# Kernel tuning notes

Measured on AMD Instinct MI355X. Metric: run time of the kernel, lower is better.

Reference implementation:

```python
import jax, jax.numpy as jnp
import numpy as np

D_MODEL = 1024
D_STATE = 16
D_CONV = 4
EXPAND = 2
D_INNER = EXPAND * D_MODEL
DT_RANK = D_MODEL // 16  # ceil(1024/16) = 64
BSZ = 2
SEQ = 1024


def _silu(x):
    return x * jax.nn.sigmoid(x)


def _mamba(x, in_proj, conv_w, conv_b, x_proj, dt_w, dt_b, A_log, Dp, out_proj):
    """Single-direction Mamba block. x: (B, L, d_model)."""
    Bb, Ll, _ = x.shape
    xz = jnp.einsum('bld,ed->ble', x, in_proj)          # (B,L,2*d_inner)
    xi, z = jnp.split(xz, 2, axis=-1)                   # (B,L,d_inner)
    # depthwise causal conv1d over L (kernel d_conv)
    xp = jnp.pad(xi, ((0, 0), (D_CONV - 1, 0), (0, 0)))
    xc = conv_b + sum(conv_w[:, k] * xp[:, k:k + Ll, :] for k in range(D_CONV))
    xc = _silu(xc)                                      # (B,L,d_inner)
    dbl = jnp.einsum('ble,fe->blf', xc, x_proj)         # (B,L,dt_rank+2*d_state)
    dt, Bm, Cm = jnp.split(dbl, [DT_RANK, DT_RANK + D_STATE], axis=-1)
    delta = jax.nn.softplus(jnp.einsum('blr,er->ble', dt, dt_w) + dt_b)  # (B,L,d_inner)
    A = -jnp.exp(A_log)                                 # (d_inner,d_state)
    dA = jnp.exp(delta[..., None] * A)                  # (B,L,E,N)
    dBu = (delta * xc)[..., None] * Bm[:, :, None, :]   # (B,L,E,N)
    def step(h, t):
        dA_t, dBu_t, C_t = t
        h = dA_t * h + dBu_t                            # (B,E,N)
        return h, jnp.einsum('ben,bn->be', h, C_t)
    h0 = jnp.zeros((Bb, D_INNER, D_STATE), x.dtype)
    _, ys = jax.lax.scan(step, h0, (dA.transpose(1, 0, 2, 3),
                                    dBu.transpose(1, 0, 2, 3),
                                    Cm.transpose(1, 0, 2)))
    y = ys.transpose(1, 0, 2) + xc * Dp                 # skip connection
    y = y * _silu(z)                                    # gate
    return jnp.einsum('ble,de->bld', y, out_proj)


def setup_inputs() -> dict:
    key = jax.random.key(0)
    ks = jax.random.split(key, 4)
    def nrm(k, shape, s=0.02):
        return s * jax.random.normal(k, shape, dtype=jnp.float32)
    def mamba_params(kb):
        k = jax.random.split(kb, 6)
        return dict(
            in_proj=nrm(k[0], (2 * D_INNER, D_MODEL)),
            conv_w=nrm(k[1], (D_INNER, D_CONV), 0.2),
            conv_b=jnp.zeros((D_INNER,), jnp.float32),
            x_proj=nrm(k[2], (DT_RANK + 2 * D_STATE, D_INNER)),
            dt_w=nrm(k[3], (D_INNER, DT_RANK), 0.1),
            dt_b=nrm(k[4], (D_INNER,), 0.5) - 4.0,  # softplus -> dt ~ 0.018
            A_log=jnp.log(jnp.broadcast_to(jnp.arange(1, D_STATE + 1, dtype=jnp.float32), (D_INNER, D_STATE))),
            D=jnp.ones((D_INNER,), jnp.float32),
            out_proj=nrm(k[5], (D_MODEL, D_INNER)),
        )
    inp = {'x': jax.random.normal(ks[2], (BSZ, SEQ, D_MODEL), dtype=jnp.float32)}
    for name, p in (('fwd', mamba_params(ks[0])), ('bwd', mamba_params(ks[1]))):
        for kk, v in p.items():
            inp[f'{name}_{kk}'] = v
    inp['merge_w'] = nrm(ks[3], (D_MODEL, 2 * D_MODEL))
    return inp


def reference(x,
              fwd_in_proj, fwd_conv_w, fwd_conv_b, fwd_x_proj, fwd_dt_w, fwd_dt_b,
              fwd_A_log, fwd_D, fwd_out_proj,
              bwd_in_proj, bwd_conv_w, bwd_conv_b, bwd_x_proj, bwd_dt_w, bwd_dt_b,
              bwd_A_log, bwd_D, bwd_out_proj,
              merge_w):
    f = _mamba(x, fwd_in_proj, fwd_conv_w, fwd_conv_b, fwd_x_proj, fwd_dt_w,
               fwd_dt_b, fwd_A_log, fwd_D, fwd_out_proj)
    b = _mamba(jnp.flip(x, 1), bwd_in_proj, bwd_conv_w, bwd_conv_b, bwd_x_proj,
               bwd_dt_w, bwd_dt_b, bwd_A_log, bwd_D, bwd_out_proj)
    b = jnp.flip(b, 1)
    return jnp.einsum('blf,df->bld', jnp.concatenate([f, b], axis=-1), merge_w)
```

## Files before the change

### kernel.cpp

```cpp
#include <hip/hip_runtime.h>
#include <math.h>

#define BSZ 2
#define SEQ 1024
#define DM  1024
#define DI  2048
#define DS  16
#define DC  4
#define DR  64
#define NDBL 96
#define NC  32
#define LC  32
#define MM  (BSZ * SEQ)

typedef unsigned short u16;
typedef __bf16 bf16x8 __attribute__((ext_vector_type(8)));
typedef float  f32x4  __attribute__((ext_vector_type(4)));

constexpr int N4_X   = MM * DM / 4;
constexpr int N4_MW  = DM * 2 * DM / 4;
constexpr int N4_IN  = 2 * DI * DM / 4;
constexpr int N4_XP  = NDBL * DI / 4;
constexpr int N4_DT  = DI * DR / 4;
constexpr int N4_OUT = DM * DI / 4;
constexpr int N4_TOTAL = N4_X + N4_MW + 2 * (N4_IN + N4_XP + N4_DT + N4_OUT);
constexpr size_t O_XP  = (size_t)2 * DI * DM;
constexpr size_t O_DT  = O_XP + (size_t)NDBL * DI;
constexpr size_t O_OUT = O_DT + (size_t)DI * DR;
constexpr size_t WBF_SZ = O_OUT + (size_t)DM * DI;

__device__ __forceinline__ u16 f2b(float f) {
    unsigned int u = __float_as_uint(f);
    unsigned int r = (u + 0x7fffu + ((u >> 16) & 1u)) >> 16;
    return (u16)r;
}
__device__ __forceinline__ float b2f(u16 h) {
    return __uint_as_float(((unsigned int)h) << 16);
}

__device__ __forceinline__ void stf(float* p, size_t i, float v) { p[i] = v; }
__device__ __forceinline__ void stf(u16* p, size_t i, float v)   { p[i] = f2b(v); }

__device__ __forceinline__ float fexp(float x)  { return __expf(x); }
__device__ __forceinline__ float frcp(float x)  { return __builtin_amdgcn_rcpf(x); }
__device__ __forceinline__ float silu_fast(float x) {
    return x * frcp(1.f + fexp(-x));
}
__device__ __forceinline__ float softplus_fast(float x) {
    return (x > 15.f) ? x : __logf(1.f + fexp(x));
}

__device__ __forceinline__ void async16(const u16* g, u16* l) {
    __builtin_amdgcn_global_load_lds(
        (const __attribute__((address_space(1))) void*)g,
        (__attribute__((address_space(3))) void*)l, 16, 0, 0);
}

__device__ __forceinline__ int lds_slot(int row, int j) {
    return row * 4 + ((j + (row >> 1)) & 3);
}

__device__ __forceinline__ void stage8f(const float* p, u16* d) {
    float4 v0 = *(const float4*)p;
    float4 v1 = *(const float4*)(p + 4);
    ushort4 a; a.x = f2b(v0.x); a.y = f2b(v0.y); a.z = f2b(v0.z); a.w = f2b(v0.w);
    ushort4 b; b.x = f2b(v1.x); b.y = f2b(v1.y); b.z = f2b(v1.z); b.w = f2b(v1.w);
    *(ushort4*)d = a;
    *(ushort4*)(d + 4) = b;
}

__global__ __launch_bounds__(256) void cvt_all_kernel(
    const float* __restrict__ s0, const float* __restrict__ s1,
    const float* __restrict__ s2, const float* __restrict__ s3,
    const float* __restrict__ s4, const float* __restrict__ s5,
    const float* __restrict__ s6, const float* __restrict__ s7,
    const float* __restrict__ s8, const float* __restrict__ s9,
    u16* __restrict__ d0, u16* __restrict__ d1, u16* __restrict__ d2,
    u16* __restrict__ d3, u16* __restrict__ d4, u16* __restrict__ d5,
    u16* __restrict__ d6, u16* __restrict__ d7, u16* __restrict__ d8,
    u16* __restrict__ d9)
{
    int i = blockIdx.x * 256 + threadIdx.x;
    const float* s; u16* d;
    if (i < N4_X) { s = s0; d = d0; }
    else if ((i -= N4_X) < N4_MW) { s = s1; d = d1; }
    else if ((i -= N4_MW) < N4_IN) { s = s2; d = d2; }
    else if ((i -= N4_IN) < N4_XP) { s = s3; d = d3; }
    else if ((i -= N4_XP) < N4_DT) { s = s4; d = d4; }
    else if ((i -= N4_DT) < N4_OUT) { s = s5; d = d5; }
    else if ((i -= N4_OUT) < N4_IN) { s = s6; d = d6; }
    else if ((i -= N4_IN) < N4_XP) { s = s7; d = d7; }
    else if ((i -= N4_XP) < N4_DT) { s = s8; d = d8; }
    else if ((i -= N4_DT) < N4_OUT) { s = s9; d = d9; }
    else return;
    float4 v = ((const float4*)s)[i];
    ushort4 o; o.x = f2b(v.x); o.y = f2b(v.y); o.z = f2b(v.z); o.w = f2b(v.w);
    ((ushort4*)d)[i] = o;
}

template <typename TA, typename TC, int ACT, bool DUAL, bool FLIP1, int NSPLIT, int BN>
__global__ __launch_bounds__(256) void mfma_gemm(
    const TA* __restrict__ A0, const TA* __restrict__ A1, int lda,
    const u16* __restrict__ W0, const u16* __restrict__ W1, int ldw,
    const float* __restrict__ bias0, const float* __restrict__ bias1,
    TC* __restrict__ C0, TC* __restrict__ C1, int ldc,
    int M, int N, int K)
{
    constexpr int NF = BN / 32;
    __shared__ u16 As[128 * 32];
    __shared__ u16 Ws[BN * 32];

    const int z = blockIdx.z;
    const int dir = DUAL ? (z / NSPLIT) : 0;
    const int split = z % NSPLIT;
    const TA* A = dir ? A1 : A0;
    const u16* W = dir ? W1 : W0;
    const float* bias = dir ? bias1 : bias0;
    TC* C = dir ? C1 : C0;
    if (NSPLIT > 1) C += (size_t)split * M * ldc;
    const int kseg = K / NSPLIT;
    const int kbeg = split * kseg, kend = kbeg + kseg;

    const int t = threadIdx.x;
    const int wave = t >> 6;
    const int lane = t & 63;
    const int wm = (wave & 1) * 64;
    const int wn = (wave >> 1) * (BN / 2);
    const int fm = lane & 15;
    const int q  = lane >> 4;
    const int m0 = blockIdx.y * 128;
    const int n0 = blockIdx.x * BN;

    f32x4 acc[4][NF] = {};

    for (int k0 = kbeg; k0 < kend; k0 += 32) {
        if constexpr (__is_same(TA, u16)) {
            #pragma unroll
            for (int p = 0; p < 2; p++) {
                int i = p * 256 + wave * 64 + lane;
                int r = i >> 2;
                int j = ((i & 3) - (r >> 1)) & 3;
                async16(A + (size_t)(m0 + r) * lda + k0 + j * 8,
                        &As[(size_t)(p * 256 + wave * 64) * 8]);
            }
        } else {
            #pragma unroll
            for (int p = 0; p < 2; p++) {
                int i = p * 256 + t;
                int r = i >> 2;
                int j = ((i & 3) - (r >> 1)) & 3;
                stage8f(A + (size_t)(m0 + r) * lda + k0 + j * 8, &As[(size_t)i * 8]);
            }
        }
        #pragma unroll
        for (int p = 0; p < BN / 64; p++) {
            int i = p * 256 + wave * 64 + lane;
            int r = i >> 2;
            int j = ((i & 3) - (r >> 1)) & 3;
            int gr = n0 + r;
            if (gr >= N) gr = N - 1;
            async16(W + (size_t)gr * ldw + k0 + j * 8,
                    &Ws[(size_t)(p * 256 + wave * 64) * 8]);
        }
        __syncthreads();

        bf16x8 af[4], wf[NF];
        #pragma unroll
        for (int mi = 0; mi < 4; mi++)
            af[mi] = *(const bf16x8*)&As[(size_t)lds_slot(wm + mi * 16 + fm, q) * 8];
        #pragma unroll
        for (int ni = 0; ni < NF; ni++)
            wf[ni] = *(const bf16x8*)&Ws[(size_t)lds_slot(wn + ni * 16 + fm, q) * 8];
        #pragma unroll
        for (int mi = 0; mi < 4; mi++)
            #pragma unroll
            for (int ni = 0; ni < NF; ni++)
                acc[mi][ni] = __builtin_amdgcn_mfma_f32_16x16x32_bf16(
                    af[mi], wf[ni], acc[mi][ni], 0, 0, 0);
        __syncthreads();
    }

    const int rb = q * 4;
    const int cc = fm;
    #pragma unroll
    for (int mi = 0; mi < 4; mi++) {
        #pragma unroll
        for (int r = 0; r < 4; r++) {
            int gm = m0 + wm + mi * 16 + rb + r;
            int om = gm;
            if (FLIP1 && dir == 1) {
                int bb = gm / SEQ, l = gm % SEQ;
                om = bb * SEQ + (SEQ - 1 - l);
            }
            #pragma unroll
            for (int ni = 0; ni < NF; ni++) {
                int gn = n0 + wn + ni * 16 + cc;
                if (gn < N) {
                    float v = acc[mi][ni][r];
                    if (ACT == 1) v = softplus_fast(v + bias[gn]);
                    stf(C, (size_t)om * ldc + gn, v);
                }
            }
        }
    }
}

__global__ __launch_bounds__(256) void combine_dbl_kernel(
    const float* __restrict__ par, float* __restrict__ dbl)
{
    int i4 = blockIdx.x * 256 + threadIdx.x;
    const int per = (MM * NDBL) / 4;
    int dir = (i4 >= per) ? 1 : 0;
    int j4 = i4 - dir * per;
    const float* p = par + (size_t)dir * 4 * MM * NDBL;
    f32x4 s = {0.f, 0.f, 0.f, 0.f};
    #pragma unroll
    for (int k = 0; k < 4; k++)
        s += *(const f32x4*)&p[(size_t)k * MM * NDBL + (size_t)j4 * 4];
    *(f32x4*)&dbl[(size_t)dir * MM * NDBL + (size_t)j4 * 4] = s;
}

__global__ __launch_bounds__(256) void combine_cat_kernel(
    const float* __restrict__ par, u16* __restrict__ cat)
{
    int i4 = blockIdx.x * 256 + threadIdx.x;
    const int per = (MM * DM) / 4;
    int dir = (i4 >= per) ? 1 : 0;
    int j4 = i4 - dir * per;
    const float* p0 = par + (size_t)dir * 2 * MM * DM;
    const float* p1 = p0 + (size_t)MM * DM;
    f32x4 a = *(const f32x4*)&p0[(size_t)j4 * 4];
    f32x4 b = *(const f32x4*)&p1[(size_t)j4 * 4];
    int m = j4 >> 8;
    int n4 = j4 & 255;
    ushort4 o;
    o.x = f2b(a[0] + b[0]); o.y = f2b(a[1] + b[1]);
    o.z = f2b(a[2] + b[2]); o.w = f2b(a[3] + b[3]);
    *(ushort4*)&cat[(size_t)m * 2 * DM + dir * DM + n4 * 4] = o;
}

__global__ __launch_bounds__(256) void combine_out_kernel(
    const float* __restrict__ p0, float* __restrict__ out)
{
    int i4 = blockIdx.x * 256 + threadIdx.x;
    const float* p1 = p0 + (size_t)MM * DM;
    f32x4 a = *(const f32x4*)&p0[(size_t)i4 * 4];
    f32x4 b = *(const f32x4*)&p1[(size_t)i4 * 4];
    *(f32x4*)&out[(size_t)i4 * 4] = a + b;
}

__global__ __launch_bounds__(256) void conv_silu_kernel(
    const float* __restrict__ xz,
    const float* __restrict__ cw0, const float* __restrict__ cw1,
    const float* __restrict__ cb0, const float* __restrict__ cb1,
    u16* __restrict__ xcb)
{
    int i4 = blockIdx.x * 256 + threadIdx.x;
    const int per = MM * DI / 4;
    int dir = (i4 >= per) ? 1 : 0;
    int rem = i4 - dir * per;
    int e4 = rem & (DI / 4 - 1);
    int bl = rem / (DI / 4);
    int l = bl & (SEQ - 1);
    int e = e4 * 4;
    const float* xz_d = xz + (size_t)dir * MM * 2 * DI;
    const float* cw = dir ? cw1 : cw0;
    const float* cb = dir ? cb1 : cb0;
    f32x4 cwv[4];
    #pragma unroll
    for (int i = 0; i < 4; i++) cwv[i] = *(const f32x4*)&cw[(e + i) * DC];
    f32x4 acc = *(const f32x4*)&cb[e];
    #pragma unroll
    for (int k = 0; k < DC; k++) {
        int ll = l + k - (DC - 1);
        if (ll >= 0) {
            f32x4 xv = *(const f32x4*)&xz_d[(size_t)(bl - l + ll) * (2 * DI) + e];
            #pragma unroll
            for (int i = 0; i < 4; i++) acc[i] += cwv[i][k] * xv[i];
        }
    }
    ushort4 o;
    #pragma unroll
    for (int i = 0; i < 4; i++) {
        float s = silu_fast(acc[i]);
        ((u16*)&o)[i] = f2b(s);
    }
    ((ushort4*)xcb)[(size_t)dir * per + rem] = o;
}

__global__ __launch_bounds__(256) void scan_pass1(
    const float* __restrict__ dbl,
    const u16*  __restrict__ xc,
    const u16*  __restrict__ delta,
    const float* __restrict__ Alog0, const float* __restrict__ Alog1,
    float* __restrict__ Pout, float* __restrict__ Qout)
{
    __shared__ float sB[LC][16];
    const int t = threadIdx.x;
    const int c = blockIdx.x;
    const int dir = blockIdx.z >> 1;
    const int b = blockIdx.z & 1;
    const int e = blockIdx.y * 256 + t;
    const int row0 = b * SEQ + c * LC;
    const float* dbl_d = dbl + (size_t)dir * MM * NDBL;
    const u16* xc_d = xc + (size_t)dir * MM * DI;
    const u16* delta_d = delta + (size_t)dir * MM * DI;
    const float* A_log = dir ? Alog1 : Alog0;
    float* P_d = Pout + (size_t)dir * BSZ * NC * DI * DS;
    float* Q_d = Qout + (size_t)dir * BSZ * NC * DI * DS;

    if (t < LC * 4) {
        int row = t >> 2, col = (t & 3) * 4;
        *(f32x4*)&sB[row][col] =
            *(const f32x4*)&dbl_d[(size_t)(row0 + row) * NDBL + DR + col];
    }

    f32x4 Aen[4], P[4], Q[4];
    #pragma unroll
    for (int g = 0; g < 4; g++) {
        f32x4 a = *(const f32x4*)&A_log[(size_t)e * DS + g * 4];
        #pragma unroll
        for (int j = 0; j < 4; j++) Aen[g][j] = -fexp(a[j]);
        P[g] = f32x4{1.f, 1.f, 1.f, 1.f};
        Q[g] = f32x4{0.f, 0.f, 0.f, 0.f};
    }
    __syncthreads();

    float dv = b2f(delta_d[(size_t)row0 * DI + e]);
    float xv = b2f(xc_d[(size_t)row0 * DI + e]);
    for (int i = 0; i < LC; i++) {
        int ip = (i + 1 < LC) ? (i + 1) : (LC - 1);
        float dvn = b2f(delta_d[(size_t)(row0 + ip) * DI + e]);
        float xvn = b2f(xc_d[(size_t)(row0 + ip) * DI + e]);
        float du = dv * xv;
        #pragma unroll
        for (int g = 0; g < 4; g++) {
            f32x4 Bv = *(const f32x4*)&sB[i][g * 4];
            #pragma unroll
            for (int j = 0; j < 4; j++) {
                float dA = fexp(dv * Aen[g][j]);
                P[g][j] *= dA;
                Q[g][j] = dA * Q[g][j] + du * Bv[j];
            }
        }
        dv = dvn; xv = xvn;
    }
    size_t base = ((size_t)(b * NC + c) * DI + e) * DS;
    #pragma unroll
    for (int g = 0; g < 4; g++) {
        *(f32x4*)&P_d[base + g * 4] = P[g];
        *(f32x4*)&Q_d[base + g * 4] = Q[g];
    }
}

__global__ __launch_bounds__(256) void scan_pass2(
    const float* __restrict__ P, const float* __restrict__ Q,
    float* __restrict__ H0)
{
    const int gid = blockIdx.x * 256 + threadIdx.x;
    const int dir = gid >> 16;
    const int loc = gid & 65535;
    const int b = loc >> 15;
    const int en = loc & (DI * DS - 1);
    size_t doff = (size_t)dir * BSZ * NC * DI * DS;
    float h = 0.f;
    for (int c = 0; c < NC; c++) {
        size_t idx = doff + ((size_t)(b * NC + c) * DI * DS) + en;
        H0[idx] = h;
        h = P[idx] * h + Q[idx];
    }
}

__global__ __launch_bounds__(256) void scan_pass3(
    const float* __restrict__ dbl,
    const u16*  __restrict__ xc,
    const float* __restrict__ xz,
    u16* delta_y,
    const float* __restrict__ Alog0, const float* __restrict__ Alog1,
    const float* __restrict__ Dp0, const float* __restrict__ Dp1,
    const float* __restrict__ H0)
{
    __shared__ float sBC[LC][32];
    const int t = threadIdx.x;
    const int c = blockIdx.x;
    const int dir = blockIdx.z >> 1;
    const int b = blockIdx.z & 1;
    const int e = blockIdx.y * 256 + t;
    const int row0 = b * SEQ + c * LC;
    const float* dbl_d = dbl + (size_t)dir * MM * NDBL;
    const u16* xc_d = xc + (size_t)dir * MM * DI;
    const float* xz_d = xz + (size_t)dir * MM * 2 * DI;
    u16* dy_d = delta_y + (size_t)dir * MM * DI;
    const float* A_log = dir ? Alog1 : Alog0;
    const float* Dp = dir ? Dp1 : Dp0;
    const float* H0_d = H0 + (size_t)dir * BSZ * NC * DI * DS;

    {
        int row = t >> 3, col = (t & 7) * 4;
        *(f32x4*)&sBC[row][col] =
            *(const f32x4*)&dbl_d[(size_t)(row0 + row) * NDBL + DR + col];
    }

    f32x4 Aen[4], h[4];
    size_t base = ((size_t)(b * NC + c) * DI + e) * DS;
    #pragma unroll
    for (int g = 0; g < 4; g++) {
        f32x4 a = *(const f32x4*)&A_log[(size_t)e * DS + g * 4];
        #pragma unroll
        for (int j = 0; j < 4; j++) Aen[g][j] = -fexp(a[j]);
        h[g] = *(const f32x4*)&H0_d[base + g * 4];
    }
    const float Dv = Dp[e];
    __syncthreads();

    float dv = b2f(dy_d[(size_t)row0 * DI + e]);
    float xv = b2f(xc_d[(size_t)row0 * DI + e]);
    float zv = xz_d[(size_t)row0 * (2 * DI) + DI + e];
    for (int i = 0; i < LC; i++) {
        int ip = (i + 1 < LC) ? (i + 1) : (LC - 1);
        float dvn = b2f(dy_d[(size_t)(row0 + ip) * DI + e]);
        float xvn = b2f(xc_d[(size_t)(row0 + ip) * DI + e]);
        float zvn = xz_d[(size_t)(row0 + ip) * (2 * DI) + DI + e];
        float du = dv * xv;
        f32x4 pv = {0.f, 0.f, 0.f, 0.f};
        #pragma unroll
        for (int g = 0; g < 4; g++) {
            f32x4 Bv = *(const f32x4*)&sBC[i][g * 4];
            f32x4 Cv = *(const f32x4*)&sBC[i][16 + g * 4];
            #pragma unroll
            for (int j = 0; j < 4; j++) {
                float dA = fexp(dv * Aen[g][j]);
                h[g][j] = dA * h[g][j] + du * Bv[j];
                pv[j] += h[g][j] * Cv[j];
            }
        }
        float p = pv[0] + pv[1] + pv[2] + pv[3];
        float y = (p + xv * Dv) * silu_fast(zv);
        dy_d[(size_t)(row0 + i) * DI + e] = f2b(y);
        dv = dvn; xv = xvn; zv = zvn;
    }
}

extern "C" void kernel_launch(void* const* d_in, const int* in_sizes, int n_in,
                              void* d_out, int out_size, void* d_ws, size_t ws_size,
                              hipStream_t stream)
{
    const float* x = (const float*)d_in[0];
    const float* in_p[2]  = {(const float*)d_in[1],  (const float*)d_in[10]};
    const float* conv_w[2]= {(const float*)d_in[2],  (const float*)d_in[11]};
    const float* conv_b[2]= {(const float*)d_in[3],  (const float*)d_in[12]};
    const float* x_p[2]   = {(const float*)d_in[4],  (const float*)d_in[13]};
    const float* dt_w[2]  = {(const float*)d_in[5],  (const float*)d_in[14]};
    const float* dt_b[2]  = {(const float*)d_in[6],  (const float*)d_in[15]};
    const float* A_log[2] = {(const float*)d_in[7],  (const float*)d_in[16]};
    const float* Dp[2]    = {(const float*)d_in[8],  (const float*)d_in[17]};
    const float* out_p[2] = {(const float*)d_in[9],  (const float*)d_in[18]};
    const float* merge_w  = (const float*)d_in[19];
    float* out = (float*)d_out;

    float* ws = (float*)d_ws;
    float* ws_xz  = ws;
    float* ws_dbl = ws_xz  + (size_t)2 * MM * 2 * DI;
    float* ws_P   = ws_dbl + (size_t)2 * MM * NDBL;
    float* ws_Q   = ws_P   + (size_t)2 * BSZ * NC * DI * DS;
    float* ws_H0  = ws_Q   + (size_t)2 * BSZ * NC * DI * DS;
    u16* ws_delta = (u16*)(ws_H0 + (size_t)2 * BSZ * NC * DI * DS);
    u16* ws_xcb   = ws_delta + (size_t)2 * MM * DI;
    u16* ws_cat   = ws_xcb   + (size_t)2 * MM * DI;
    u16* ws_xbf   = ws_cat   + (size_t)MM * 2 * DM;
    u16* wbf_mw   = ws_xbf   + (size_t)MM * DM;
    u16* wbf0     = wbf_mw   + (size_t)DM * 2 * DM;
    u16* wbf1     = wbf0     + WBF_SZ;
    float* ws_par = ws_P;

    cvt_all_kernel<<<(N4_TOTAL + 255) / 256, 256, 0, stream>>>(
        x, merge_w, in_p[0], x_p[0], dt_w[0], out_p[0],
        in_p[1], x_p[1], dt_w[1], out_p[1],
        ws_xbf, wbf_mw,
        wbf0, wbf0 + O_XP, wbf0 + O_DT, wbf0 + O_OUT,
        wbf1, wbf1 + O_XP, wbf1 + O_DT, wbf1 + O_OUT);

    mfma_gemm<u16, float, 0, true, true, 1, 128><<<dim3(32, 16, 2), 256, 0, stream>>>(
        ws_xbf, ws_xbf, DM, wbf0, wbf1, DM, nullptr, nullptr,
        ws_xz, ws_xz + (size_t)MM * 2 * DI, 2 * DI, MM, 2 * DI, DM);

    conv_silu_kernel<<<(2 * MM * DI / 4) / 256, 256, 0, stream>>>(
        ws_xz, conv_w[0], conv_w[1], conv_b[0], conv_b[1], ws_xcb);

    mfma_gemm<u16, float, 0, true, false, 4, 64><<<dim3(2, 16, 8), 256, 0, stream>>>(
        ws_xcb, ws_xcb + (size_t)MM * DI, DI,
        wbf0 + O_XP, wbf1 + O_XP, DI, nullptr, nullptr,
        ws_par, ws_par + (size_t)4 * MM * NDBL, NDBL, MM, NDBL, DI);
    combine_dbl_kernel<<<(2 * MM * NDBL / 4) / 256, 256, 0, stream>>>(ws_par, ws_dbl);

    mfma_gemm<float, u16, 1, true, false, 1, 64><<<dim3(32, 16, 2), 256, 0, stream>>>(
        ws_dbl, ws_dbl + (size_t)MM * NDBL, NDBL,
        wbf0 + O_DT, wbf1 + O_DT, DR, dt_b[0], dt_b[1],
        ws_delta, ws_delta + (size_t)MM * DI, DI, MM, DI, DR);

    {
        dim3 grid(NC, DI / 256, 2 * BSZ);
        scan_pass1<<<grid, 256, 0, stream>>>(ws_dbl, ws_xcb, ws_delta,
                                             A_log[0], A_log[1], ws_P, ws_Q);
        scan_pass2<<<(2 * BSZ * DI * DS) / 256, 256, 0, stream>>>(ws_P, ws_Q, ws_H0);
        scan_pass3<<<grid, 256, 0, stream>>>(ws_dbl, ws_xcb, ws_xz, ws_delta,
                                             A_log[0], A_log[1], Dp[0], Dp[1], ws_H0);
    }

    mfma_gemm<u16, float, 0, true, true, 2, 64><<<dim3(16, 16, 4), 256, 0, stream>>>(
        ws_delta, ws_delta + (size_t)MM * DI, DI,
        wbf0 + O_OUT, wbf1 + O_OUT, DI, nullptr, nullptr,
        ws_par, ws_par + (size_t)2 * MM * DM, DM, MM, DM, DI);
    combine_cat_kernel<<<(2 * MM * DM / 4) / 256, 256, 0, stream>>>(ws_par, ws_cat);

    mfma_gemm<u16, float, 0, false, false, 2, 64><<<dim3(16, 16, 2), 256, 0, stream>>>(
        ws_cat, ws_cat, 2 * DM, wbf_mw, wbf_mw, 2 * DM, nullptr, nullptr,
        ws_par, ws_par, DM, MM, DM, 2 * DM);
    combine_out_kernel<<<(MM * DM / 4) / 256, 256, 0, stream>>>(ws_par, out);
}
```

Measured before the change: 395.8 us.

## Replace in_proj GEMM with 256x256-tile double-buffered async-LDS MFMA kernel

Adds a dedicated in_proj GEMM kernel that uses 256x256 output tiles, 512 threads, 128 KB of LDS with swizzled layout, async global-to-LDS loads and double buffering interleaved with 16x16x32 bf16 MFMAs. It is meant to raise operand reuse and overlap loads with math compared to the older 128-wide tile GEMM for the largest projection. The tradeoff is that only 256 blocks are launched, which may underfill the GPU. Heavy LDS use also limits occupancy to one block per CU, and the manual waitcnt schedule is fragile.

```diff
diff --git a/kernel.cpp b/kernel.cpp
--- a/kernel.cpp
+++ b/kernel.cpp
@@ -98,6 +98,179 @@
     ((ushort4*)d)[i] = o;
 }
 
+__global__ __launch_bounds__(512) void gemm256_dual(
+    const u16* __restrict__ A,
+    const u16* __restrict__ Wd0, const u16* __restrict__ Wd1,
+    float* __restrict__ Cd0, float* __restrict__ Cd1,
+    int lda, int ldw, int ldc, int K)
+{
+    __shared__ u16 lds[65536];
+    const int t    = threadIdx.x;
+    const int lane = t & 63;
+    const int w    = t >> 6;
+    const int wr   = w >> 2;
+    const int wc   = w & 3;
+    const int fm   = lane & 15;
+    const int q    = lane >> 4;
+    const int dir  = blockIdx.z;
+    const u16* W   = dir ? Wd1 : Wd0;
+    float* C       = dir ? Cd1 : Cd0;
+    const int m0   = blockIdx.y * 256;
+    const int n0   = blockIdx.x * 256;
+    const int T    = K >> 6;
+
+    int offA[4][2], offW[2][2];
+    #pragma unroll
+    for (int mi = 0; mi < 4; mi++)
+        #pragma unroll
+        for (int kk = 0; kk < 2; kk++) {
+            int r = wr * 64 + mi * 16 + fm;
+            int j = kk * 4 + q;
+            offA[mi][kk] = (r * 8 + ((j + r) & 7)) * 8;
+        }
+    #pragma unroll
+    for (int ni = 0; ni < 2; ni++)
+        #pragma unroll
+        for (int kk = 0; kk < 2; kk++) {
+            int r = wc * 32 + ni * 16 + fm;
+            int j = kk * 4 + q;
+            offW[ni][kk] = (r * 8 + ((j + r) & 7)) * 8;
+        }
+
+    int sr[2], sj[2];
+    #pragma unroll
+    for (int p = 0; p < 2; p++) {
+        int slot = p * 512 + t;
+        sr[p] = slot >> 3;
+        sj[p] = ((slot & 7) - sr[p]) & 7;
+    }
+    const int ldsWaveBase = (t & ~63) * 8;
+
+#define STAGE(G, ld, row0, kcol, dstBase)                                    \
+    { _Pragma("unroll")                                                      \
+      for (int p = 0; p < 2; p++) {                                          \
+          const u16* src_ = (G) + (size_t)((row0) + sr[p]) * (ld)            \
+                          + (kcol) + sj[p] * 8;                              \
+          async16(src_, &lds[(dstBase) + p * 4096 + ldsWaveBase]);           \
+      } }
+
+    f32x4 acc[2][2][4][2] = {};
+    bf16x8 af[4][2], wf[2][2];
+
+#define DSREAD_A(mh, cur)                                                    \
+    { _Pragma("unroll")                                                      \
+      for (int mi = 0; mi < 4; mi++)                                         \
+          _Pragma("unroll")                                                  \
+          for (int kk = 0; kk < 2; kk++)                                     \
+              af[mi][kk] = *(const bf16x8*)&lds[(cur) + (mh) * 8192          \
+                                                + offA[mi][kk]]; }
+#define DSREAD_W(nh, cur)                                                    \
+    { _Pragma("unroll")                                                      \
+      for (int ni = 0; ni < 2; ni++)                                         \
+          _Pragma("unroll")                                                  \
+          for (int kk = 0; kk < 2; kk++)                                     \
+              wf[ni][kk] = *(const bf16x8*)&lds[(cur) + 16384 + (nh) * 8192  \
+                                                + offW[ni][kk]]; }
+#define MFMA16(mh, nh)                                                       \
+    { __builtin_amdgcn_s_setprio(1);                                         \
+      _Pragma("unroll")                                                      \
+      for (int mi = 0; mi < 4; mi++)                                         \
+          _Pragma("unroll")                                                  \
+          for (int ni = 0; ni < 2; ni++)                                     \
+              _Pragma("unroll")                                              \
+              for (int kk = 0; kk < 2; kk++)                                 \
+                  acc[mh][nh][mi][ni] =                                      \
+                      __builtin_amdgcn_mfma_f32_16x16x32_bf16(               \
+                          af[mi][kk], wf[ni][kk], acc[mh][nh][mi][ni],       \
+                          0, 0, 0);                                          \
+      __builtin_amdgcn_s_setprio(0); }
+
+#define WAITVM(n) asm volatile("s_waitcnt vmcnt(" #n ")" ::: "memory")
+#define BAR() __builtin_amdgcn_s_barrier()
+
+    STAGE(A, lda, m0,       0, 0);
+    STAGE(W, ldw, n0,       0, 16384);
+    STAGE(W, ldw, n0 + 128, 0, 16384 + 8192);
+    STAGE(A, lda, m0 + 128, 0, 8192);
+    WAITVM(4);
+    BAR();
+
+    for (int tt = 0; tt < T - 1; ++tt) {
+        const int cur = (tt & 1) * 32768;
+        const int nxt = 32768 - cur;
+        const int kn  = (tt + 1) << 6;
+        DSREAD_A(0, cur); DSREAD_W(0, cur);
+        STAGE(A, lda, m0, kn, nxt);
+        WAITVM(4);
+        BAR();
+        MFMA16(0, 0);
+        BAR();
+        DSREAD_W(1, cur);
+        STAGE(W, ldw, n0, kn, nxt + 16384);
+        WAITVM(4);
+        BAR();
+        MFMA16(0, 1);
+        BAR();
+        DSREAD_A(1, cur);
+        STAGE(W, ldw, n0 + 128, kn, nxt + 16384 + 8192);
+        BAR();
+        MFMA16(1, 1);
+        BAR();
+        DSREAD_W(0, cur);
+        STAGE(A, lda, m0 + 128, kn, nxt + 8192);
+        WAITVM(4);
+        BAR();
+        MFMA16(1, 0);
+        BAR();
+    }
+    {
+        const int cur = ((T - 1) & 1) * 32768;
+        DSREAD_A(0, cur); DSREAD_W(0, cur);
+        WAITVM(2);
+        BAR();
+        MFMA16(0, 0);
+        BAR();
+        DSREAD_W(1, cur);
+        WAITVM(0);
+        BAR();
+        MFMA16(0, 1);
+        BAR();
+        DSREAD_A(1, cur);
+        BAR();
+        MFMA16(1, 1);
+        BAR();
+        DSREAD_W(0, cur);
+        MFMA16(1, 0);
+    }
+#undef STAGE
+#undef DSREAD_A
+#undef DSREAD_W
+#undef MFMA16
+#undef WAITVM
+#undef BAR
+
+    #pragma unroll
+    for (int mh = 0; mh < 2; mh++)
+        #pragma unroll
+        for (int mi = 0; mi < 4; mi++)
+            #pragma unroll
+            for (int rr = 0; rr < 4; rr++) {
+                int gm = m0 + mh * 128 + wr * 64 + mi * 16 + q * 4 + rr;
+                int om = gm;
+                if (dir == 1) {
+                    om = (gm & ~(SEQ - 1)) | ((SEQ - 1) - (gm & (SEQ - 1)));
+                }
+                float* crow = C + (size_t)om * ldc;
+                #pragma unroll
+                for (int nh = 0; nh < 2; nh++)
+                    #pragma unroll
+                    for (int ni = 0; ni < 2; ni++) {
+                        int gn = n0 + nh * 128 + wc * 32 + ni * 16 + fm;
+                        crow[gn] = acc[mh][nh][mi][ni][rr];
+                    }
+            }
+}
+
 template <typename TA, typename TC, int ACT, bool DUAL, bool FLIP1, int NSPLIT, int BN>
 __global__ __launch_bounds__(256) void mfma_gemm(
     const TA* __restrict__ A0, const TA* __restrict__ A1, int lda,
@@ -480,9 +653,10 @@
         wbf0, wbf0 + O_XP, wbf0 + O_DT, wbf0 + O_OUT,
         wbf1, wbf1 + O_XP, wbf1 + O_DT, wbf1 + O_OUT);
 
-    mfma_gemm<u16, float, 0, true, true, 1, 128><<<dim3(32, 16, 2), 256, 0, stream>>>(
-        ws_xbf, ws_xbf, DM, wbf0, wbf1, DM, nullptr, nullptr,
-        ws_xz, ws_xz + (size_t)MM * 2 * DI, 2 * DI, MM, 2 * DI, DM);
+    gemm256_dual<<<dim3(16, 8, 2), 512, 0, stream>>>(
+        ws_xbf, wbf0, wbf1,
+        ws_xz, ws_xz + (size_t)MM * 2 * DI,
+        DM, DM, 2 * DI, DM);
 
     conv_silu_kernel<<<(2 * MM * DI / 4) / 256, 256, 0, stream>>>(
         ws_xz, conv_w[0], conv_w[1], conv_b[0], conv_b[1], ws_xcb);
```

Result: faster. 375.7 us (-5.1%).
